# Kernel tuning notes

Hardware: AMD Instinct MI355X
Metric: run time of the kernel (lower is better)

The kernel has to match this reference:

```python
import jax, jax.numpy as jnp
import numpy as np

N_NODES = 50000
N_EDGES = 800000
N_GRAPHS = 1024
IN_DIM, HID, OUT_DIM = 78, 256, 128
EPS = 1e-5


def setup_inputs() -> dict:
    key = jax.random.key(0)
    ks = jax.random.split(key, 12)
    def lin(k, fi, fo):
        s = 1.0 / np.sqrt(fi)
        return jax.random.uniform(k, (fi, fo), jnp.float32, -s, s)
    inp = {
        "x_l": jax.random.normal(ks[0], (N_NODES, IN_DIM), jnp.float32),
        "edge_index_l": jax.random.randint(ks[1], (2, N_EDGES), 0, N_NODES, jnp.int64),
        "batch_l": jnp.sort(jax.random.randint(ks[2], (N_NODES,), 0, N_GRAPHS, jnp.int64)),
        # GraphConv 1: 78 -> 256 (lin_rel has bias, lin_root no bias)
        "W1_rel": lin(ks[3], IN_DIM, HID), "b1_rel": jnp.zeros((HID,), jnp.float32), "W1_root": lin(ks[4], IN_DIM, HID),
        # GraphConv 2: 256 -> 512
        "W2_rel": lin(ks[5], HID, 2 * HID), "b2_rel": jnp.zeros((2 * HID,), jnp.float32), "W2_root": lin(ks[6], HID, 2 * HID),
        # GraphConv 3: 512 -> 512
        "W3_rel": lin(ks[7], 2 * HID, 2 * HID), "b3_rel": jnp.zeros((2 * HID,), jnp.float32), "W3_root": lin(ks[8], 2 * HID, 2 * HID),
        # fc1: Linear(512 -> 128) + LayerNorm(128); Dropout(0.01) is identity in eval
        "W_fc": lin(ks[9], 2 * HID, OUT_DIM), "b_fc": jnp.zeros((OUT_DIM,), jnp.float32),
        "ln_g": jnp.ones((OUT_DIM,), jnp.float32), "ln_b": jnp.zeros((OUT_DIM,), jnp.float32),
    }
    return inp


def _graph_conv(x, src, dst, W_rel, b_rel, W_root):
    # PyG GraphConv (aggr='add'): out = lin_rel(sum_{j->i} x_j) + lin_root(x_i)
    aggr = jax.ops.segment_sum(x[src], dst, num_segments=x.shape[0])  # [N, d_in]
    return aggr @ W_rel + b_rel + x @ W_root


def reference(x_l, edge_index_l, batch_l,
              W1_rel, b1_rel, W1_root,
              W2_rel, b2_rel, W2_root,
              W3_rel, b3_rel, W3_root,
              W_fc, b_fc, ln_g, ln_b):
    src, dst = edge_index_l[0], edge_index_l[1]
    h = jax.nn.relu(_graph_conv(x_l, src, dst, W1_rel, b1_rel, W1_root))
    h = jax.nn.relu(_graph_conv(h, src, dst, W2_rel, b2_rel, W2_root))
    h = jax.nn.relu(_graph_conv(h, src, dst, W3_rel, b3_rel, W3_root))
    # fc1: Linear -> LayerNorm -> Dropout(0.01, identity in eval) -> ReLU
    z = h @ W_fc + b_fc
    mu = jnp.mean(z, axis=-1, keepdims=True)
    var = jnp.mean(jnp.square(z - mu), axis=-1, keepdims=True)
    z = (z - mu) * jax.lax.rsqrt(var + EPS) * ln_g + ln_b
    x_atom = jax.nn.relu(z)  # [N, OUT_DIM]
    pooled = jax.ops.segment_sum(x_atom, batch_l, num_segments=N_GRAPHS)  # [G, OUT_DIM]
    return (x_atom, pooled)
```

## Files before the change

kernel.cpp:

```cpp
#include <hip/hip_runtime.h>

#define N_NODES 50000
#define N_EDGES 800000
#define N_GRAPHS 1024
#define IN_DIM 78
#define K1P 96
#define HID 256
#define OUT_DIM 128

typedef unsigned short ushort_t;
typedef __attribute__((ext_vector_type(8))) short v8s;
typedef __attribute__((ext_vector_type(4))) float v4f;
typedef __attribute__((ext_vector_type(4))) unsigned int u4;
typedef __attribute__((ext_vector_type(2))) unsigned short us2;
typedef __attribute__((ext_vector_type(4))) unsigned short us4;
typedef __attribute__((ext_vector_type(8))) unsigned short us8;

__device__ __forceinline__ ushort_t f2bf(float f) {
    unsigned u = __float_as_uint(f);
    unsigned r = (u + 0x7fffu + ((u >> 16) & 1u)) >> 16;
    return (ushort_t)r;
}
__device__ __forceinline__ float bf2f(ushort_t h) {
    return __uint_as_float((unsigned)h << 16);
}

__global__ __launch_bounds__(256)
void wt_all_kernel(const float* __restrict__ W1r, const float* __restrict__ W1o,
                   const float* __restrict__ W2r, const float* __restrict__ W2o,
                   const float* __restrict__ W3r, const float* __restrict__ W3o,
                   const float* __restrict__ Wfc, ushort_t* __restrict__ out)
{
    int i = blockIdx.x * 256 + threadIdx.x;
    if (i >= 901120) return;
    const float* W; int K, N, Kp, base;
    if      (i < 24576)  { W = W1r; K = IN_DIM; N = HID;     Kp = 96;  base = 0; }
    else if (i < 49152)  { W = W1o; K = IN_DIM; N = HID;     Kp = 96;  base = 24576; }
    else if (i < 180224) { W = W2r; K = HID;    N = 2 * HID; Kp = 256; base = 49152; }
    else if (i < 311296) { W = W2o; K = HID;    N = 2 * HID; Kp = 256; base = 180224; }
    else if (i < 573440) { W = W3r; K = 2*HID;  N = 2 * HID; Kp = 512; base = 311296; }
    else if (i < 835584) { W = W3o; K = 2*HID;  N = 2 * HID; Kp = 512; base = 573440; }
    else                 { W = Wfc; K = 2*HID;  N = OUT_DIM; Kp = 512; base = 835584; }
    int j = i - base;
    int n = j / Kp, k = j - n * Kp;
    float v = (k < K) ? W[(size_t)k * N + n] : 0.0f;
    out[i] = f2bf(v);
}

__global__ __launch_bounds__(256)
void pad_cast_kernel(const float* __restrict__ in, ushort_t* __restrict__ out,
                     int rows, int Kin, int Kout)
{
    int i = blockIdx.x * 256 + threadIdx.x;
    if (i >= rows * Kout) return;
    int r = i / Kout, k = i - r * Kout;
    out[i] = f2bf(k < Kin ? in[(size_t)r * Kin + k] : 0.0f);
}

__global__ __launch_bounds__(256)
void hist_kernel(const int* __restrict__ dstI, int* __restrict__ deg, int nE)
{
    int e = blockIdx.x * 256 + threadIdx.x;
    if (e < nE) {
        int d = dstI[e];
        if ((unsigned)d < (unsigned)N_NODES) atomicAdd(&deg[d], 1);
    }
}

__global__ __launch_bounds__(1024)
void scan1_kernel(const int* __restrict__ deg, int* __restrict__ rowptr,
                  int* __restrict__ blocksum, int n)
{
    __shared__ int s[1024];
    int b = (int)blockIdx.x, t = (int)threadIdx.x;
    int i = b * 1024 + t;
    int v = (i < n) ? deg[i] : 0;
    s[t] = v;
    __syncthreads();
    for (int off = 1; off < 1024; off <<= 1) {
        int a = (t >= off) ? s[t - off] : 0;
        __syncthreads();
        s[t] += a;
        __syncthreads();
    }
    if (i < n) rowptr[i + 1] = s[t];
    if (t == 1023) blocksum[b] = s[1023];
    if (b == 0 && t == 0) rowptr[0] = 0;
}

__global__ __launch_bounds__(64)
void scan2_kernel(int* __restrict__ blocksum, int nb)
{
    int t = (int)threadIdx.x;
    int v = (t < nb) ? blocksum[t] : 0;
    #pragma unroll
    for (int off = 1; off < 64; off <<= 1) {
        int a = __shfl_up(v, off, 64);
        if (t >= off) v += a;
    }
    if (t < nb) blocksum[t] = v;
}

__global__ __launch_bounds__(256)
void scan3_kernel(const int* __restrict__ blocksum, int* __restrict__ rowptr,
                  int* __restrict__ cursor, int n)
{
    int j = blockIdx.x * 256 + threadIdx.x;
    if (j > n) return;
    int v;
    if (j == 0) v = 0;
    else {
        int b = (j - 1) >> 10;
        v = rowptr[j] + (b >= 1 ? blocksum[b - 1] : 0);
    }
    rowptr[j] = v;
    if (j < n) cursor[j] = v;
}

__global__ __launch_bounds__(256)
void fill_kernel(const int* __restrict__ srcI, const int* __restrict__ dstI,
                 int* __restrict__ cursor, int* __restrict__ csr_src, int nE)
{
    int e = blockIdx.x * 256 + threadIdx.x;
    if (e < nE) {
        int d = dstI[e];
        int s = srcI[e];
        if ((unsigned)d < (unsigned)N_NODES && (unsigned)s < (unsigned)N_NODES) {
            int pos = atomicAdd(&cursor[d], 1);
            csr_src[pos] = s;
        }
    }
}

template<int VPT> struct VecT;
template<> struct VecT<2> { using T = us2; };
template<> struct VecT<4> { using T = us4; };
template<> struct VecT<8> { using T = us8; };

template<int VPT>
__global__ __launch_bounds__(256)
void csr_agg_wave_kernel(const ushort_t* __restrict__ feat,
                         const int* __restrict__ rowptr,
                         const int* __restrict__ csr_src,
                         ushort_t* __restrict__ out, int Ds)
{
    using T = typename VecT<VPT>::T;
    const int wv   = (int)threadIdx.x >> 6;
    const int node = (int)blockIdx.x * 4 + wv;
    if (node >= N_NODES) return;
    const int lane = (int)threadIdx.x & 63;
    const int off0 = lane * VPT;
    const bool act = off0 < Ds;
    const int off  = act ? off0 : (Ds - VPT);

    const int e0 = rowptr[node], e1 = rowptr[node + 1];
    float acc[VPT];
    #pragma unroll
    for (int i = 0; i < VPT; ++i) acc[i] = 0.0f;

    int e = e0;
    for (; e + 8 <= e1; e += 8) {
        T r[8];
        #pragma unroll
        for (int u = 0; u < 8; ++u) {
            int s = csr_src[e + u];
            r[u] = *(const T*)(feat + (size_t)s * Ds + off);
        }
        #pragma unroll
        for (int u = 0; u < 8; ++u)
            #pragma unroll
            for (int i = 0; i < VPT; ++i) acc[i] += bf2f(r[u][i]);
    }
    for (; e + 4 <= e1; e += 4) {
        T r[4];
        #pragma unroll
        for (int u = 0; u < 4; ++u) {
            int s = csr_src[e + u];
            r[u] = *(const T*)(feat + (size_t)s * Ds + off);
        }
        #pragma unroll
        for (int u = 0; u < 4; ++u)
            #pragma unroll
            for (int i = 0; i < VPT; ++i) acc[i] += bf2f(r[u][i]);
    }
    for (; e < e1; ++e) {
        int s = csr_src[e];
        T r = *(const T*)(feat + (size_t)s * Ds + off);
        #pragma unroll
        for (int i = 0; i < VPT; ++i) acc[i] += bf2f(r[i]);
    }

    if (act) {
        T o;
        #pragma unroll
        for (int i = 0; i < VPT; ++i) o[i] = f2bf(acc[i]);
        *(T*)(out + (size_t)node * Ds + off0) = o;
    }
}

template<int NT>
__global__ __launch_bounds__(256, 2)
void mfma_gemm_kernel(const ushort_t* __restrict__ A1,
                      const ushort_t* __restrict__ A2,
                      const ushort_t* __restrict__ W1t,
                      const ushort_t* __restrict__ W2t,
                      const float* __restrict__ bias,
                      void* __restrict__ outp,
                      int M, int K, int Fo, int relu, int out_bf16)
{
    constexpr int BN    = NT * 32;
    constexpr int NBT   = NT * 2;
    constexpr int BT_PW = NBT / 4;
    __shared__ __align__(16) ushort_t Al[8 * 512];
    __shared__ __align__(16) ushort_t Bl[NBT * 512];
    const int tid = (int)threadIdx.x;
    const int l   = tid & 63;
    const int w   = tid >> 6;
    const int q   = l >> 4;
    const int r15 = l & 15;
    const int bm  = blockIdx.y * 128;
    const int bn  = blockIdx.x * BN;
    const int wm  = w >> 1, wn = w & 1;

    const int s1 = K >> 5;
    const int nsteps = A2 ? (2 * s1) : s1;

    v4f acc[4][NT];
    #pragma unroll
    for (int mt = 0; mt < 4; ++mt)
        #pragma unroll
        for (int nt = 0; nt < NT; ++nt)
            acc[mt][nt] = (v4f){0.0f, 0.0f, 0.0f, 0.0f};

    u4 ra[2], rb[BT_PW];
    auto load_step = [&](int step) {
        const ushort_t* A  = (step >= s1) ? A2  : A1;
        const ushort_t* Bt = (step >= s1) ? W2t : W1t;
        const int k0 = ((step >= s1) ? (step - s1) : step) << 5;
        #pragma unroll
        for (int ii = 0; ii < 2; ++ii) {
            int it  = w * 2 + ii;
            int row = bm + it * 16 + r15;
            if (row < M) ra[ii] = *(const u4*)(A + (size_t)row * K + k0 + q * 8);
            else         ra[ii] = (u4){0u, 0u, 0u, 0u};
        }
        #pragma unroll
        for (int jj = 0; jj < BT_PW; ++jj) {
            int jt  = w * BT_PW + jj;
            int col = bn + jt * 16 + r15;
            rb[jj] = *(const u4*)(Bt + (size_t)col * K + k0 + q * 8);
        }
    };

    load_step(0);
    for (int step = 0; step < nsteps; ++step) {
        __syncthreads();
        #pragma unroll
        for (int ii = 0; ii < 2; ++ii)
            *(u4*)(Al + (size_t)(w * 2 + ii) * 512 + l * 8) = ra[ii];
        #pragma unroll
        for (int jj = 0; jj < BT_PW; ++jj)
            *(u4*)(Bl + (size_t)(w * BT_PW + jj) * 512 + l * 8) = rb[jj];
        if (step + 1 < nsteps) load_step(step + 1);
        __syncthreads();
        v8s af[4], bf[NT];
        #pragma unroll
        for (int mt = 0; mt < 4; ++mt)
            af[mt] = *(const v8s*)(Al + (size_t)(wm * 4 + mt) * 512 + l * 8);
        #pragma unroll
        for (int nt = 0; nt < NT; ++nt)
            bf[nt] = *(const v8s*)(Bl + (size_t)(wn * NT + nt) * 512 + l * 8);
        #pragma unroll
        for (int mt = 0; mt < 4; ++mt)
            #pragma unroll
            for (int nt = 0; nt < NT; ++nt)
                acc[mt][nt] = __builtin_amdgcn_mfma_f32_16x16x32_bf16(
                    af[mt], bf[nt], acc[mt][nt], 0, 0, 0);
    }

    #pragma unroll
    for (int nt = 0; nt < NT; ++nt) {
        int col = bn + wn * (NT * 16) + nt * 16 + r15;
        float bb = bias[col];
        #pragma unroll
        for (int mt = 0; mt < 4; ++mt) {
            #pragma unroll
            for (int p = 0; p < 4; ++p) {
                int row = bm + wm * 64 + mt * 16 + q * 4 + p;
                if (row < M) {
                    float v = acc[mt][nt][p] + bb;
                    if (relu) v = fmaxf(v, 0.0f);
                    if (out_bf16) ((ushort_t*)outp)[(size_t)row * Fo + col] = f2bf(v);
                    else          ((float*)outp)[(size_t)row * Fo + col]   = v;
                }
            }
        }
    }
}

__global__ __launch_bounds__(128)
void ln_relu_pool_kernel(const float* __restrict__ z,
                         const float* __restrict__ gamma,
                         const float* __restrict__ beta,
                         const int* __restrict__ batch,
                         float* __restrict__ x_atom,
                         float* __restrict__ pooled)
{
    int row = (int)blockIdx.x;
    int t = (int)threadIdx.x;
    float v = z[(long long)row * 128 + t];

    __shared__ float red[2];
    float s = v;
    #pragma unroll
    for (int o = 32; o >= 1; o >>= 1) s += __shfl_xor(s, o, 64);
    int wave = t >> 6;
    if ((t & 63) == 0) red[wave] = s;
    __syncthreads();
    float mean = (red[0] + red[1]) * (1.0f / 128.0f);

    float d = v - mean;
    float s2 = d * d;
    #pragma unroll
    for (int o = 32; o >= 1; o >>= 1) s2 += __shfl_xor(s2, o, 64);
    __syncthreads();
    if ((t & 63) == 0) red[wave] = s2;
    __syncthreads();
    float var = (red[0] + red[1]) * (1.0f / 128.0f);

    float y = d * rsqrtf(var + 1e-5f) * gamma[t] + beta[t];
    y = fmaxf(y, 0.0f);
    x_atom[(long long)row * 128 + t] = y;
    int b = batch[row];
    if ((unsigned)b < (unsigned)N_GRAPHS)
        atomicAdd(pooled + (long long)b * 128 + t, y);
}

extern "C" void kernel_launch(void* const* d_in, const int* in_sizes, int n_in,
                              void* d_out, int out_size, void* d_ws, size_t ws_size,
                              hipStream_t stream)
{
    const float* x     = (const float*)d_in[0];
    const int*   ei    = (const int*)d_in[1];
    const int*   batch = (const int*)d_in[2];
    const float* W1r   = (const float*)d_in[3];
    const float* b1    = (const float*)d_in[4];
    const float* W1o   = (const float*)d_in[5];
    const float* W2r   = (const float*)d_in[6];
    const float* b2    = (const float*)d_in[7];
    const float* W2o   = (const float*)d_in[8];
    const float* W3r   = (const float*)d_in[9];
    const float* b3    = (const float*)d_in[10];
    const float* W3o   = (const float*)d_in[11];
    const float* Wfc   = (const float*)d_in[12];
    const float* bfc   = (const float*)d_in[13];
    const float* lng   = (const float*)d_in[14];
    const float* lnb   = (const float*)d_in[15];

    const size_t WS_NEED = 204800000;
    if (ws_size < WS_NEED) {
        hipMemsetAsync(d_out, 0, (size_t)out_size * sizeof(float), stream);
        return;
    }

    char* ws = (char*)d_ws;
    ushort_t* xb   = (ushort_t*)(ws + 0);
    ushort_t* h1   = (ushort_t*)(ws + 9600000);
    float*    z    = (float*)   (ws + 0);
    ushort_t* aggr = (ushort_t*)(ws + 35200000);
    ushort_t* h2   = (ushort_t*)(ws + 86400000);
    ushort_t* h3   = (ushort_t*)(ws + 137600000);
    int* deg    = (int*)(ws + 188800000);
    int* rowptr = (int*)(ws + 189000000);
    int* cursor = (int*)(ws + 189200128);
    int* csrsrc = (int*)(ws + 189400128);
    int* blksum = (int*)(ws + 192600128);
    ushort_t* wt = (ushort_t*)(ws + 192600512);
    ushort_t* w1r_t = wt;
    ushort_t* w1o_t = wt + 24576;
    ushort_t* w2r_t = wt + 49152;
    ushort_t* w2o_t = wt + 180224;
    ushort_t* w3r_t = wt + 311296;
    ushort_t* w3o_t = wt + 573440;
    ushort_t* wfc_t = wt + 835584;

    float* x_atom = (float*)d_out;
    float* pooled = x_atom + (size_t)N_NODES * OUT_DIM;

    const int* src = ei;
    const int* dst = ei + N_EDGES;

    wt_all_kernel<<<(901120 + 255) / 256, 256, 0, stream>>>(W1r, W1o, W2r, W2o,
                                                            W3r, W3o, Wfc, wt);
    pad_cast_kernel<<<((N_NODES * K1P) + 255) / 256, 256, 0, stream>>>(x, xb, N_NODES, IN_DIM, K1P);

    hipMemsetAsync(deg, 0, N_NODES * sizeof(int), stream);
    hist_kernel<<<(N_EDGES + 255) / 256, 256, 0, stream>>>(dst, deg, N_EDGES);
    {
        int nb = (N_NODES + 1023) / 1024;
        scan1_kernel<<<nb, 1024, 0, stream>>>(deg, rowptr, blksum, N_NODES);
        scan2_kernel<<<1, 64, 0, stream>>>(blksum, nb);
        scan3_kernel<<<(N_NODES + 1 + 255) / 256, 256, 0, stream>>>(blksum, rowptr, cursor, N_NODES);
    }
    fill_kernel<<<(N_EDGES + 255) / 256, 256, 0, stream>>>(src, dst, cursor, csrsrc, N_EDGES);

    const int GY = (N_NODES + 127) / 128;
    const int AGG_BLKS = (N_NODES + 3) / 4;

    csr_agg_wave_kernel<2><<<AGG_BLKS, 256, 0, stream>>>(xb, rowptr, csrsrc, aggr, K1P);
    {
        dim3 g(HID / 256, GY);
        mfma_gemm_kernel<8><<<g, 256, 0, stream>>>(aggr, xb, w1r_t, w1o_t, b1, h1,
                                                   N_NODES, K1P, HID, 1, 1);
    }
    csr_agg_wave_kernel<4><<<AGG_BLKS, 256, 0, stream>>>(h1, rowptr, csrsrc, aggr, HID);
    {
        dim3 g((2 * HID) / 256, GY);
        mfma_gemm_kernel<8><<<g, 256, 0, stream>>>(aggr, h1, w2r_t, w2o_t, b2, h2,
                                                   N_NODES, HID, 2 * HID, 1, 1);
    }
    csr_agg_wave_kernel<8><<<AGG_BLKS, 256, 0, stream>>>(h2, rowptr, csrsrc, aggr, 2 * HID);
    {
        dim3 g((2 * HID) / 256, GY);
        mfma_gemm_kernel<8><<<g, 256, 0, stream>>>(aggr, h2, w3r_t, w3o_t, b3, h3,
                                                   N_NODES, 2 * HID, 2 * HID, 1, 1);
    }
    {
        dim3 g(OUT_DIM / 128, GY);
        mfma_gemm_kernel<4><<<g, 256, 0, stream>>>(h3, nullptr, wfc_t, nullptr, bfc, z,
                                                   N_NODES, 2 * HID, OUT_DIM, 0, 0);
    }
    hipMemsetAsync(pooled, 0, (size_t)N_GRAPHS * OUT_DIM * sizeof(float), stream);
    ln_relu_pool_kernel<<<N_NODES, 128, 0, stream>>>(z, lng, lnb, batch, x_atom, pooled);
}
```

Baseline: 705.2 us.

## Rework GEMM with direct global-to-LDS loads, double buffering, and staged bf16 stores

```diff
diff --git a/kernel.cpp b/kernel.cpp
--- a/kernel.cpp
+++ b/kernel.cpp
@@ -23,6 +23,12 @@
 }
 __device__ __forceinline__ float bf2f(ushort_t h) {
     return __uint_as_float((unsigned)h << 16);
+}
+
+__device__ __forceinline__ void gload16(const ushort_t* g, ushort_t* l) {
+    __builtin_amdgcn_global_load_lds(
+        (const __attribute__((address_space(1))) void*)g,
+        (__attribute__((address_space(3))) void*)l, 16, 0, 0);
 }
 
 __global__ __launch_bounds__(256)
@@ -198,8 +204,7 @@
     }
 }
 
-template<int NT>
-__global__ __launch_bounds__(256, 2)
+__global__ __launch_bounds__(256, 3)
 void mfma_gemm_kernel(const ushort_t* __restrict__ A1,
                       const ushort_t* __restrict__ A2,
                       const ushort_t* __restrict__ W1t,
@@ -208,90 +213,115 @@
                       void* __restrict__ outp,
                       int M, int K, int Fo, int relu, int out_bf16)
 {
-    constexpr int BN    = NT * 32;
-    constexpr int NBT   = NT * 2;
-    constexpr int BT_PW = NBT / 4;
-    __shared__ __align__(16) ushort_t Al[8 * 512];
-    __shared__ __align__(16) ushort_t Bl[NBT * 512];
+    __shared__ __align__(16) ushort_t smem[17408];
     const int tid = (int)threadIdx.x;
     const int l   = tid & 63;
     const int w   = tid >> 6;
     const int q   = l >> 4;
     const int r15 = l & 15;
     const int bm  = blockIdx.y * 128;
-    const int bn  = blockIdx.x * BN;
+    const int bn  = blockIdx.x * 128;
     const int wm  = w >> 1, wn = w & 1;
 
     const int s1 = K >> 5;
     const int nsteps = A2 ? (2 * s1) : s1;
 
-    v4f acc[4][NT];
-    #pragma unroll
-    for (int mt = 0; mt < 4; ++mt)
-        #pragma unroll
-        for (int nt = 0; nt < NT; ++nt)
-            acc[mt][nt] = (v4f){0.0f, 0.0f, 0.0f, 0.0f};
-
-    u4 ra[2], rb[BT_PW];
-    auto load_step = [&](int step) {
+    int aOff[2], bOff[2];
+    #pragma unroll
+    for (int ii = 0; ii < 2; ++ii) {
+        int ar = bm + (w * 2 + ii) * 16 + r15;
+        if (ar >= M) ar = M - 1;
+        aOff[ii] = ar * K;
+        int bc = bn + (w * 2 + ii) * 16 + r15;
+        bOff[ii] = bc * K;
+    }
+    const int kq = q * 8;
+
+    auto stage = [&](int step, int buf) {
         const ushort_t* A  = (step >= s1) ? A2  : A1;
         const ushort_t* Bt = (step >= s1) ? W2t : W1t;
-        const int k0 = ((step >= s1) ? (step - s1) : step) << 5;
-        #pragma unroll
-        for (int ii = 0; ii < 2; ++ii) {
-            int it  = w * 2 + ii;
-            int row = bm + it * 16 + r15;
-            if (row < M) ra[ii] = *(const u4*)(A + (size_t)row * K + k0 + q * 8);
-            else         ra[ii] = (u4){0u, 0u, 0u, 0u};
-        }
-        #pragma unroll
-        for (int jj = 0; jj < BT_PW; ++jj) {
-            int jt  = w * BT_PW + jj;
-            int col = bn + jt * 16 + r15;
-            rb[jj] = *(const u4*)(Bt + (size_t)col * K + k0 + q * 8);
-        }
+        const int k0 = (((step >= s1) ? (step - s1) : step) << 5) + kq;
+        ushort_t* db = smem + buf * 8192;
+        #pragma unroll
+        for (int ii = 0; ii < 2; ++ii)
+            gload16(A + aOff[ii] + k0, db + (size_t)(w * 2 + ii) * 512);
+        #pragma unroll
+        for (int ii = 0; ii < 2; ++ii)
+            gload16(Bt + bOff[ii] + k0, db + (size_t)(8 + w * 2 + ii) * 512);
     };
 
-    load_step(0);
+    v4f acc[4][4];
+    #pragma unroll
+    for (int mt = 0; mt < 4; ++mt)
+        #pragma unroll
+        for (int nt = 0; nt < 4; ++nt)
+            acc[mt][nt] = (v4f){0.0f, 0.0f, 0.0f, 0.0f};
+
+    stage(0, 0);
     for (int step = 0; step < nsteps; ++step) {
+        const int cur = step & 1;
         __syncthreads();
-        #pragma unroll
-        for (int ii = 0; ii < 2; ++ii)
-            *(u4*)(Al + (size_t)(w * 2 + ii) * 512 + l * 8) = ra[ii];
-        #pragma unroll
-        for (int jj = 0; jj < BT_PW; ++jj)
-            *(u4*)(Bl + (size_t)(w * BT_PW + jj) * 512 + l * 8) = rb[jj];
-        if (step + 1 < nsteps) load_step(step + 1);
-        __syncthreads();
-        v8s af[4], bf[NT];
+        if (step + 1 < nsteps) stage(step + 1, cur ^ 1);
+        const ushort_t* db = smem + cur * 8192;
+        v8s af[4], bf[4];
         #pragma unroll
         for (int mt = 0; mt < 4; ++mt)
-            af[mt] = *(const v8s*)(Al + (size_t)(wm * 4 + mt) * 512 + l * 8);
-        #pragma unroll
-        for (int nt = 0; nt < NT; ++nt)
-            bf[nt] = *(const v8s*)(Bl + (size_t)(wn * NT + nt) * 512 + l * 8);
+            af[mt] = *(const v8s*)(db + (size_t)(wm * 4 + mt) * 512 + l * 8);
+        #pragma unroll
+        for (int nt = 0; nt < 4; ++nt)
+            bf[nt] = *(const v8s*)(db + (size_t)(8 + wn * 4 + nt) * 512 + l * 8);
         #pragma unroll
         for (int mt = 0; mt < 4; ++mt)
             #pragma unroll
-            for (int nt = 0; nt < NT; ++nt)
+            for (int nt = 0; nt < 4; ++nt)
                 acc[mt][nt] = __builtin_amdgcn_mfma_f32_16x16x32_bf16(
                     af[mt], bf[nt], acc[mt][nt], 0, 0, 0);
     }
 
-    #pragma unroll
-    for (int nt = 0; nt < NT; ++nt) {
-        int col = bn + wn * (NT * 16) + nt * 16 + r15;
-        float bb = bias[col];
-        #pragma unroll
-        for (int mt = 0; mt < 4; ++mt) {
+    if (out_bf16) {
+        __syncthreads();
+        #pragma unroll
+        for (int nt = 0; nt < 4; ++nt) {
+            int col = wn * 64 + nt * 16 + r15;
+            float bb = bias[bn + col];
             #pragma unroll
-            for (int p = 0; p < 4; ++p) {
-                int row = bm + wm * 64 + mt * 16 + q * 4 + p;
-                if (row < M) {
+            for (int mt = 0; mt < 4; ++mt) {
+                int row0 = wm * 64 + mt * 16 + q * 4;
+                #pragma unroll
+                for (int p = 0; p < 4; ++p) {
                     float v = acc[mt][nt][p] + bb;
                     if (relu) v = fmaxf(v, 0.0f);
-                    if (out_bf16) ((ushort_t*)outp)[(size_t)row * Fo + col] = f2bf(v);
-                    else          ((float*)outp)[(size_t)row * Fo + col]   = v;
+                    smem[(size_t)(row0 + p) * 136 + col] = f2bf(v);
+                }
+            }
+        }
+        __syncthreads();
+        ushort_t* op = (ushort_t*)outp;
+        #pragma unroll
+        for (int pass = 0; pass < 8; ++pass) {
+            int row = pass * 16 + (tid >> 4);
+            int gr  = bm + row;
+            if (gr < M) {
+                u4 v = *(const u4*)(smem + (size_t)row * 136 + (tid & 15) * 8);
+                *(u4*)(op + (size_t)gr * Fo + bn + (tid & 15) * 8) = v;
+            }
+        }
+    } else {
+        float* op = (float*)outp;
+        #pragma unroll
+        for (int nt = 0; nt < 4; ++nt) {
+            int col = bn + wn * 64 + nt * 16 + r15;
+            float bb = bias[col];
+            #pragma unroll
+            for (int mt = 0; mt < 4; ++mt) {
+                #pragma unroll
+                for (int p = 0; p < 4; ++p) {
+                    int row = bm + wm * 64 + mt * 16 + q * 4 + p;
+                    if (row < M) {
+                        float v = acc[mt][nt][p] + bb;
+                        if (relu) v = fmaxf(v, 0.0f);
+                        op[(size_t)row * Fo + col] = v;
+                    }
                 }
             }
         }
@@ -409,26 +439,26 @@
 
     csr_agg_wave_kernel<2><<<AGG_BLKS, 256, 0, stream>>>(xb, rowptr, csrsrc, aggr, K1P);
     {
-        dim3 g(HID / 256, GY);
-        mfma_gemm_kernel<8><<<g, 256, 0, stream>>>(aggr, xb, w1r_t, w1o_t, b1, h1,
-                                                   N_NODES, K1P, HID, 1, 1);
+        dim3 g(HID / 128, GY);
+        mfma_gemm_kernel<<<g, 256, 0, stream>>>(aggr, xb, w1r_t, w1o_t, b1, h1,
+                                                N_NODES, K1P, HID, 1, 1);
     }
     csr_agg_wave_kernel<4><<<AGG_BLKS, 256, 0, stream>>>(h1, rowptr, csrsrc, aggr, HID);
     {
-        dim3 g((2 * HID) / 256, GY);
-        mfma_gemm_kernel<8><<<g, 256, 0, stream>>>(aggr, h1, w2r_t, w2o_t, b2, h2,
-                                                   N_NODES, HID, 2 * HID, 1, 1);
+        dim3 g((2 * HID) / 128, GY);
+        mfma_gemm_kernel<<<g, 256, 0, stream>>>(aggr, h1, w2r_t, w2o_t, b2, h2,
+                                                N_NODES, HID, 2 * HID, 1, 1);
     }
     csr_agg_wave_kernel<8><<<AGG_BLKS, 256, 0, stream>>>(h2, rowptr, csrsrc, aggr, 2 * HID);
     {
-        dim3 g((2 * HID) / 256, GY);
-        mfma_gemm_kernel<8><<<g, 256, 0, stream>>>(aggr, h2, w3r_t, w3o_t, b3, h3,
-                                                   N_NODES, 2 * HID, 2 * HID, 1, 1);
+        dim3 g((2 * HID) / 128, GY);
+        mfma_gemm_kernel<<<g, 256, 0, stream>>>(aggr, h2, w3r_t, w3o_t, b3, h3,
+                                                N_NODES, 2 * HID, 2 * HID, 1, 1);
     }
     {
         dim3 g(OUT_DIM / 128, GY);
-        mfma_gemm_kernel<4><<<g, 256, 0, stream>>>(h3, nullptr, wfc_t, nullptr, bfc, z,
-                                                   N_NODES, 2 * HID, OUT_DIM, 0, 0);
+        mfma_gemm_kernel<<<g, 256, 0, stream>>>(h3, nullptr, wfc_t, nullptr, bfc, z,
+                                                N_NODES, 2 * HID, OUT_DIM, 0, 0);
     }
     hipMemsetAsync(pooled, 0, (size_t)N_GRAPHS * OUT_DIM * sizeof(float), stream);
     ln_relu_pool_kernel<<<N_NODES, 128, 0, stream>>>(z, lng, lnb, batch, x_atom, pooled);
```

Measured after the change: 651.4 us. -7.6%, faster.
